# Kernel optimization log

Measured on AMD Instinct MI355X. Metric: run time of the kernel, lower is better.

The kernel has to match this reference:

```python
import jax, jax.numpy as jnp
import numpy as np

F_DIM = 2
L_LEVELS = 16
N_MIN, N_MAX = 16, 2048
_B = np.exp((np.log(N_MAX) - np.log(N_MIN)) / (L_LEVELS - 1))
NL = np.array([int(np.floor(N_MIN * _B ** l)) for l in range(L_LEVELS)], dtype=np.float32)
T_SIZE = 2 ** 19
AABB = 3.0
N_PTS = 262144
N_FREQ_DIR = 4  # direction PE frequencies -> 3 + 3*2*4 = 27 dims (matches color_MLP input 16+27)
PIS = np.array([1, 2654435761, 805459861], dtype=np.uint32)
# 8 cube-corner offsets; order matches the torch vertex enumeration
OFFS = np.array([[0,0,0],[1,0,0],[0,1,0],[1,1,0],[0,0,1],[1,0,1],[0,1,1],[1,1,1]], dtype=np.float32)


def _hash_encode(xn, tables):
    # xn: [N,3] normalized positions in ~[0,1); tables: [L,T,F]
    Ns = jnp.asarray(NL)                                   # [L]
    scaled = xn[None, :, :] * Ns[:, None, None]            # [L,N,3]
    fl = jnp.floor(scaled)
    loc = scaled - fl                                      # [L,N,3] trilinear weights
    offs_i = jnp.asarray(OFFS, jnp.int32)                  # [8,3]
    verts = fl.astype(jnp.int32)[:, :, None, :] + offs_i[None, None]   # [L,N,8,3]
    v = verts.astype(jnp.uint32)
    pis = jnp.asarray(PIS)
    h = ((v[..., 0] * pis[0]) ^ (v[..., 1] * pis[1]) ^ (v[..., 2] * pis[2])) % jnp.uint32(T_SIZE)
    idx = h.astype(jnp.int32)                              # [L,N,8]
    corner = jax.vmap(lambda t, i: t[i])(tables, idx)      # [L,N,8,F] hashed gather
    offs = jnp.asarray(OFFS)                               # [8,3]
    w = jnp.prod(offs[None, None] * loc[:, :, None, :] + (1.0 - offs[None, None]) * (1.0 - loc[:, :, None, :]), axis=-1)  # [L,N,8]
    feats = jnp.einsum('lnc,lncf->lnf', w, corner)         # [L,N,F]
    N = xn.shape[0]
    return feats.transpose(1, 0, 2).reshape(N, L_LEVELS * F_DIM)  # [N, L*F]


def _pos_enc_dir(d):
    outs = [d]
    for j in range(N_FREQ_DIR):
        outs.append(jnp.sin((2.0 ** j) * d))
        outs.append(jnp.cos((2.0 ** j) * d))
    return jnp.concatenate(outs, axis=1)                   # [N,27]


def setup_inputs() -> dict:
    key = jax.random.key(0)
    ks = jax.random.split(key, 12)
    x = jax.random.normal(ks[0], (N_PTS, 3), jnp.float32)
    d = jax.random.normal(ks[1], (N_PTS, 3), jnp.float32)
    tables = (jax.random.uniform(ks[2], (L_LEVELS, T_SIZE, F_DIM), jnp.float32) * 2.0 - 1.0) * 1e-4
    def lin(k, fi, fo):
        return jax.random.normal(k, (fi, fo), jnp.float32) * (1.0 / np.sqrt(fi))
    return {
        'x': x, 'd': d, 'tables': tables,
        'dW1': lin(ks[3], 32, 64), 'db1': jnp.zeros((64,), jnp.float32),
        'dW2': lin(ks[4], 64, 16), 'db2': jnp.zeros((16,), jnp.float32),
        'cW1': lin(ks[5], 43, 64), 'cb1': jnp.zeros((64,), jnp.float32),
        'cW2': lin(ks[6], 64, 64), 'cb2': jnp.zeros((64,), jnp.float32),
        'cW3': lin(ks[7], 64, 3), 'cb3': jnp.zeros((3,), jnp.float32),
    }


def reference(x, d, tables, dW1, db1, dW2, db2, cW1, cb1, cW2, cb2, cW3, cb3):
    xn = x / AABB
    mask = (jnp.abs(xn[:, 0]) < 0.5) & (jnp.abs(xn[:, 1]) < 0.5) & (jnp.abs(xn[:, 2]) < 0.5)
    xn = xn + 0.5
    feats = _hash_encode(xn, tables)                        # [N,32]
    h = jnp.maximum(feats @ dW1 + db1, 0.0) @ dW2 + db2     # [N,16]
    d_enc = _pos_enc_dir(d)                                 # [N,27]
    ch = jnp.concatenate([h, d_enc], axis=1)                # [N,43]
    ch = jnp.maximum(ch @ cW1 + cb1, 0.0)
    ch = jnp.maximum(ch @ cW2 + cb2, 0.0)
    rgb = jax.nn.sigmoid(ch @ cW3 + cb3)                    # [N,3]
    sigma = jnp.where(mask, h[:, 0], jnp.float32(-100000.0))
    rgb = jnp.where(mask[:, None], rgb, 0.0)
    return rgb, jnp.exp(sigma)
```

## Files before the change

kernel.cpp:

```cpp
#include <hip/hip_runtime.h>

#define NPTS 262144
#define HP1 2654435761u
#define HP2 805459861u
#define TMASK 0x7FFFFu

typedef __attribute__((ext_vector_type(8))) short short8;
typedef __attribute__((ext_vector_type(4))) float f32x4;
typedef unsigned short ushort_t;
typedef unsigned int uint_t;

#define MFMA(a, b, c) __builtin_amdgcn_mfma_f32_16x16x32_bf16((a), (b), (c), 0, 0, 0)

__device__ __forceinline__ ushort_t f2bf(float f) {
    uint_t u = __float_as_uint(f);
    return (ushort_t)((u + 0x7FFFu + ((u >> 16) & 1u)) >> 16);
}
__device__ __forceinline__ float sigmoidf_fast(float v) {
    return 1.0f / (1.0f + __expf(-v));
}

#define DOFF0 0
#define DOFF1 4913
#define DOFF2 17080
#define DOFF3 46871
#define DOFF4 126378
#define DTOT  331757
#define DENSE_BLOCKS 1296

#define WS_DN_OFF (16u * 1024u * 1024u)
#define WS_WF_OFF (22u * 1024u * 1024u)

#define OFF_DW1 0
#define OFF_DW2 2048
#define OFF_CW1 3072
#define OFF_CW2 7168
#define OFF_CW3 11264
#define WF_TOTAL 12288
#define PREP_BLOCKS 48

extern "C" __global__ void ngp_predense(
    const float* __restrict__ dW1, const float* __restrict__ dW2,
    const float* __restrict__ cW1, const float* __restrict__ cW2,
    const float* __restrict__ cW3, ushort_t* __restrict__ wf,
    const float* __restrict__ tbl, f32x4* __restrict__ dense)
{
    if (blockIdx.x < PREP_BLOCKS) {
        const int e = blockIdx.x * 256 + (int)threadIdx.x;
        if (e >= WF_TOTAL) return;
        const float* W; int base, NT, KR, NR;
        if (e < OFF_DW2)      { W = dW1; base = OFF_DW1; NT = 4; KR = 32; NR = 64; }
        else if (e < OFF_CW1) { W = dW2; base = OFF_DW2; NT = 1; KR = 64; NR = 16; }
        else if (e < OFF_CW2) { W = cW1; base = OFF_CW1; NT = 4; KR = 43; NR = 64; }
        else if (e < OFF_CW3) { W = cW2; base = OFF_CW2; NT = 4; KR = 64; NR = 64; }
        else                  { W = cW3; base = OFF_CW3; NT = 1; KR = 64; NR = 3;  }
        const int r = e - base;
        const int frag = r >> 9;
        const int lane = (r >> 3) & 63;
        const int j = r & 7;
        const int kc = frag / NT, nt = frag % NT;
        const int k = kc * 32 + ((lane >> 4) << 3) + j;
        const int n = nt * 16 + (lane & 15);
        const float v = (k < KR && n < NR) ? W[k * NR + n] : 0.0f;
        wf[e] = f2bf(v);
        return;
    }
    const int e = (blockIdx.x - PREP_BLOCKS) * 256 + (int)threadIdx.x;
    if (e >= DTOT) return;
    int l, base, dim;
    if (e < DOFF1)      { l = 0; base = DOFF0; dim = 17; }
    else if (e < DOFF2) { l = 1; base = DOFF1; dim = 23; }
    else if (e < DOFF3) { l = 2; base = DOFF2; dim = 31; }
    else if (e < DOFF4) { l = 3; base = DOFF3; dim = 43; }
    else                { l = 4; base = DOFF4; dim = 59; }
    const int r = e - base;
    const int v0 = r % dim;
    const int t  = r / dim;
    const int v1 = t % dim;
    const int v2 = t / dim;
    const float2* tp = (const float2*)tbl + ((size_t)l << 19);
    const unsigned hy = (unsigned)v1 * HP1;
    const unsigned hz = (unsigned)v2 * HP2;
    const unsigned h0 = ((unsigned)v0 ^ hy ^ hz) & TMASK;
    const unsigned h1 = (((unsigned)v0 + 1u) ^ hy ^ hz) & TMASK;
    const float2 c0 = tp[h0];
    const float2 c1 = tp[h1];
    dense[e] = (f32x4){c0.x, c0.y, c1.x, c1.y};
}

extern "C" __global__ void __launch_bounds__(256) ngp_encode(
    const float* __restrict__ xin, const float* __restrict__ tbl,
    const f32x4* __restrict__ dense, uint_t* __restrict__ feats)
{
    const int b  = blockIdx.x;
    const int l  = b >> 10;
    const int pt = ((b & 1023) << 8) + (int)threadIdx.x;

    static const float NLs[16] = {16.f, 22.f, 30.f, 42.f, 58.f, 80.f, 111.f, 153.f,
                                  212.f, 294.f, 406.f, 561.f, 776.f, 1072.f, 1482.f, 2048.f};
    static const int DDIM[5] = {17, 23, 31, 43, 59};
    static const int DOFFS[5] = {DOFF0, DOFF1, DOFF2, DOFF3, DOFF4};

    const float x0 = xin[3 * pt + 0];
    const float x1 = xin[3 * pt + 1];
    const float x2 = xin[3 * pt + 2];
    const bool msk = (fabsf(x0) < 1.5f) & (fabsf(x1) < 1.5f) & (fabsf(x2) < 1.5f);
    if (!msk) return;

    const float nl = NLs[l];
    const float s0 = (x0 / 3.0f + 0.5f) * nl;
    const float s1 = (x1 / 3.0f + 0.5f) * nl;
    const float s2 = (x2 / 3.0f + 0.5f) * nl;
    const float f0 = floorf(s0), f1 = floorf(s1), f2 = floorf(s2);
    const float l0 = s0 - f0, l1 = s1 - f1, l2 = s2 - f2;
    const float m0 = 1.0f - l0, m1 = 1.0f - l1, m2 = 1.0f - l2;

    float a = 0.0f, bb = 0.0f;

    if (l < 5) {
        const int dim = DDIM[l];
        const f32x4* dp = dense + DOFFS[l];
        const int idx = ((int)f2 * dim + (int)f1) * dim + (int)f0;
        const f32x4 C00 = dp[idx];
        const f32x4 C10 = dp[idx + dim];
        const f32x4 C01 = dp[idx + dim * dim];
        const f32x4 C11 = dp[idx + dim * dim + dim];
        float w;
        w = m1 * m2; a = fmaf(m0 * w, C00[0], a); bb = fmaf(m0 * w, C00[1], bb);
                     a = fmaf(l0 * w, C00[2], a); bb = fmaf(l0 * w, C00[3], bb);
        w = l1 * m2; a = fmaf(m0 * w, C10[0], a); bb = fmaf(m0 * w, C10[1], bb);
                     a = fmaf(l0 * w, C10[2], a); bb = fmaf(l0 * w, C10[3], bb);
        w = m1 * l2; a = fmaf(m0 * w, C01[0], a); bb = fmaf(m0 * w, C01[1], bb);
                     a = fmaf(l0 * w, C01[2], a); bb = fmaf(l0 * w, C01[3], bb);
        w = l1 * l2; a = fmaf(m0 * w, C11[0], a); bb = fmaf(m0 * w, C11[1], bb);
                     a = fmaf(l0 * w, C11[2], a); bb = fmaf(l0 * w, C11[3], bb);
    } else {
        const float2* tp = (const float2*)tbl + ((size_t)l << 19);
        const unsigned va0 = (unsigned)(int)f0, vb0 = va0 + 1u;
        const unsigned va1 = (unsigned)(int)f1 * HP1, vb1 = va1 + HP1;
        const unsigned va2 = (unsigned)(int)f2 * HP2, vb2 = va2 + HP2;
        const float2 c0 = tp[(va0 ^ va1 ^ va2) & TMASK];
        const float2 c1 = tp[(vb0 ^ va1 ^ va2) & TMASK];
        const float2 c2 = tp[(va0 ^ vb1 ^ va2) & TMASK];
        const float2 c3 = tp[(vb0 ^ vb1 ^ va2) & TMASK];
        const float2 c4 = tp[(va0 ^ va1 ^ vb2) & TMASK];
        const float2 c5 = tp[(vb0 ^ va1 ^ vb2) & TMASK];
        const float2 c6 = tp[(va0 ^ vb1 ^ vb2) & TMASK];
        const float2 c7 = tp[(vb0 ^ vb1 ^ vb2) & TMASK];
        float w;
        w = m1 * m2; a = fmaf(m0 * w, c0.x, a); bb = fmaf(m0 * w, c0.y, bb);
                     a = fmaf(l0 * w, c1.x, a); bb = fmaf(l0 * w, c1.y, bb);
        w = l1 * m2; a = fmaf(m0 * w, c2.x, a); bb = fmaf(m0 * w, c2.y, bb);
                     a = fmaf(l0 * w, c3.x, a); bb = fmaf(l0 * w, c3.y, bb);
        w = m1 * l2; a = fmaf(m0 * w, c4.x, a); bb = fmaf(m0 * w, c4.y, bb);
                     a = fmaf(l0 * w, c5.x, a); bb = fmaf(l0 * w, c5.y, bb);
        w = l1 * l2; a = fmaf(m0 * w, c6.x, a); bb = fmaf(m0 * w, c6.y, bb);
                     a = fmaf(l0 * w, c7.x, a); bb = fmaf(l0 * w, c7.y, bb);
    }

    feats[(size_t)l * NPTS + pt] = (uint_t)f2bf(a) | ((uint_t)f2bf(bb) << 16);
}

extern "C" __global__ void __launch_bounds__(64) ngp_mlp(
    const float* __restrict__ xin, const float* __restrict__ din,
    const uint_t* __restrict__ featsbf, const ushort_t* __restrict__ wf,
    const float* __restrict__ db1, const float* __restrict__ db2,
    const float* __restrict__ cb1, const float* __restrict__ cb2,
    const float* __restrict__ cb3,
    float* __restrict__ out)
{
    __shared__ short act[4096];
    __shared__ float mk[64];

    const int lane = (int)threadIdx.x;
    const int lrow = lane & 15;
    const int lq   = lane >> 4;
    const int ptb  = blockIdx.x * 64;
    const int p    = ptb + lane;
    char* Ab = (char*)&act[0];

#define LDSA(mt, kc) (*reinterpret_cast<const short8*>(Ab + ((((mt) * 16 + lrow) * 128 + (kc) * 64 + lq * 16) ^ ((lrow & 7) << 4))))
#define LOADB(off)   (*reinterpret_cast<const short8*>(wf + (off) + lane * 8))
#define STB16(row, col, val) *reinterpret_cast<ushort_t*>(Ab + ((((row) * 128 + (col) * 2)) ^ (((row) & 7) << 4))) = (val)

    const float x0 = xin[3 * p + 0];
    const float x1 = xin[3 * p + 1];
    const float x2 = xin[3 * p + 2];
    const bool msk = (fabsf(x0) < 1.5f) & (fabsf(x1) < 1.5f) & (fabsf(x2) < 1.5f);
    mk[lane] = msk ? 1.0f : 0.0f;

    uint_t u[16];
    #pragma unroll
    for (int l = 0; l < 16; ++l) u[l] = featsbf[(size_t)l * NPTS + p];
    #pragma unroll
    for (int c = 0; c < 4; ++c) {
        short8 v;
        #pragma unroll
        for (int q = 0; q < 4; ++q) {
            v[2 * q + 0] = (short)(u[4 * c + q] & 0xFFFFu);
            v[2 * q + 1] = (short)(u[4 * c + q] >> 16);
        }
        const int byte = (lane * 128 + 16 * c) ^ ((lane & 7) << 4);
        *reinterpret_cast<short8*>(Ab + byte) = v;
    }
    const float d0v = din[3 * p + 0];
    const float d1v = din[3 * p + 1];
    const float d2v = din[3 * p + 2];

    __syncthreads();

    f32x4 acc[4][4];
    #pragma unroll
    for (int nt = 0; nt < 4; ++nt) {
        const float b = db1[nt * 16 + lrow];
        #pragma unroll
        for (int mt = 0; mt < 4; ++mt) acc[mt][nt] = (f32x4){b, b, b, b};
    }
    {
        short8 a0 = LDSA(0, 0), a1 = LDSA(1, 0), a2 = LDSA(2, 0), a3 = LDSA(3, 0);
        #pragma unroll
        for (int nt = 0; nt < 4; ++nt) {
            const short8 B = LOADB(OFF_DW1 + nt * 512);
            acc[0][nt] = MFMA(a0, B, acc[0][nt]);
            acc[1][nt] = MFMA(a1, B, acc[1][nt]);
            acc[2][nt] = MFMA(a2, B, acc[2][nt]);
            acc[3][nt] = MFMA(a3, B, acc[3][nt]);
        }
    }
    __syncthreads();
    #pragma unroll
    for (int mt = 0; mt < 4; ++mt)
        #pragma unroll
        for (int nt = 0; nt < 4; ++nt)
            #pragma unroll
            for (int r = 0; r < 4; ++r) {
                const int row = mt * 16 + lq * 4 + r;
                STB16(row, nt * 16 + lrow, f2bf(fmaxf(acc[mt][nt][r], 0.0f)));
            }
    __syncthreads();

    f32x4 hD[4];
    {
        const float b = db2[lrow];
        #pragma unroll
        for (int mt = 0; mt < 4; ++mt) hD[mt] = (f32x4){b, b, b, b};
        #pragma unroll
        for (int kc = 0; kc < 2; ++kc) {
            const short8 B = LOADB(OFF_DW2 + kc * 512);
            #pragma unroll
            for (int mt = 0; mt < 4; ++mt) hD[mt] = MFMA(LDSA(mt, kc), B, hD[mt]);
        }
    }
    __syncthreads();

    if (lrow == 0) {
        #pragma unroll
        for (int mt = 0; mt < 4; ++mt)
            #pragma unroll
            for (int r = 0; r < 4; ++r) {
                const int row = mt * 16 + lq * 4 + r;
                out[3 * NPTS + ptb + row] = (mk[row] != 0.0f) ? __expf(hD[mt][r]) : 0.0f;
            }
    }
    #pragma unroll
    for (int mt = 0; mt < 4; ++mt)
        #pragma unroll
        for (int r = 0; r < 4; ++r) {
            const int row = mt * 16 + lq * 4 + r;
            STB16(row, lrow, f2bf(hD[mt][r]));
        }
    {
        ushort_t t[48];
        t[0] = f2bf(d0v); t[1] = f2bf(d1v); t[2] = f2bf(d2v);
        #pragma unroll
        for (int j = 0; j < 4; ++j) {
            const float s = (float)(1 << j);
            t[3 + 6 * j + 0] = f2bf(__sinf(s * d0v));
            t[3 + 6 * j + 1] = f2bf(__sinf(s * d1v));
            t[3 + 6 * j + 2] = f2bf(__sinf(s * d2v));
            t[3 + 6 * j + 3] = f2bf(__cosf(s * d0v));
            t[3 + 6 * j + 4] = f2bf(__cosf(s * d1v));
            t[3 + 6 * j + 5] = f2bf(__cosf(s * d2v));
        }
        #pragma unroll
        for (int i = 27; i < 48; ++i) t[i] = 0;
        #pragma unroll
        for (int c = 0; c < 6; ++c) {
            short8 v;
            #pragma unroll
            for (int j = 0; j < 8; ++j) v[j] = (short)t[8 * c + j];
            const int byte = (lane * 128 + 32 + 16 * c) ^ ((lane & 7) << 4);
            *reinterpret_cast<short8*>(Ab + byte) = v;
        }
    }
    __syncthreads();

    #pragma unroll
    for (int nt = 0; nt < 4; ++nt) {
        const float b = cb1[nt * 16 + lrow];
        #pragma unroll
        for (int mt = 0; mt < 4; ++mt) acc[mt][nt] = (f32x4){b, b, b, b};
    }
    #pragma unroll
    for (int kc = 0; kc < 2; ++kc) {
        short8 a0 = LDSA(0, kc), a1 = LDSA(1, kc), a2 = LDSA(2, kc), a3 = LDSA(3, kc);
        #pragma unroll
        for (int nt = 0; nt < 4; ++nt) {
            const short8 B = LOADB(OFF_CW1 + (kc * 4 + nt) * 512);
            acc[0][nt] = MFMA(a0, B, acc[0][nt]);
            acc[1][nt] = MFMA(a1, B, acc[1][nt]);
            acc[2][nt] = MFMA(a2, B, acc[2][nt]);
            acc[3][nt] = MFMA(a3, B, acc[3][nt]);
        }
    }
    __syncthreads();
    #pragma unroll
    for (int mt = 0; mt < 4; ++mt)
        #pragma unroll
        for (int nt = 0; nt < 4; ++nt)
            #pragma unroll
            for (int r = 0; r < 4; ++r) {
                const int row = mt * 16 + lq * 4 + r;
                STB16(row, nt * 16 + lrow, f2bf(fmaxf(acc[mt][nt][r], 0.0f)));
            }
    __syncthreads();

    #pragma unroll
    for (int nt = 0; nt < 4; ++nt) {
        const float b = cb2[nt * 16 + lrow];
        #pragma unroll
        for (int mt = 0; mt < 4; ++mt) acc[mt][nt] = (f32x4){b, b, b, b};
    }
    #pragma unroll
    for (int kc = 0; kc < 2; ++kc) {
        short8 a0 = LDSA(0, kc), a1 = LDSA(1, kc), a2 = LDSA(2, kc), a3 = LDSA(3, kc);
        #pragma unroll
        for (int nt = 0; nt < 4; ++nt) {
            const short8 B = LOADB(OFF_CW2 + (kc * 4 + nt) * 512);
            acc[0][nt] = MFMA(a0, B, acc[0][nt]);
            acc[1][nt] = MFMA(a1, B, acc[1][nt]);
            acc[2][nt] = MFMA(a2, B, acc[2][nt]);
            acc[3][nt] = MFMA(a3, B, acc[3][nt]);
        }
    }
    __syncthreads();
    #pragma unroll
    for (int mt = 0; mt < 4; ++mt)
        #pragma unroll
        for (int nt = 0; nt < 4; ++nt)
            #pragma unroll
            for (int r = 0; r < 4; ++r) {
                const int row = mt * 16 + lq * 4 + r;
                STB16(row, nt * 16 + lrow, f2bf(fmaxf(acc[mt][nt][r], 0.0f)));
            }
    __syncthreads();

    f32x4 rD[4];
    {
        const float b = (lrow < 3) ? cb3[lrow] : 0.0f;
        #pragma unroll
        for (int mt = 0; mt < 4; ++mt) rD[mt] = (f32x4){b, b, b, b};
        #pragma unroll
        for (int kc = 0; kc < 2; ++kc) {
            const short8 B = LOADB(OFF_CW3 + kc * 512);
            #pragma unroll
            for (int mt = 0; mt < 4; ++mt) rD[mt] = MFMA(LDSA(mt, kc), B, rD[mt]);
        }
    }
    if (lrow < 3) {
        #pragma unroll
        for (int mt = 0; mt < 4; ++mt)
            #pragma unroll
            for (int r = 0; r < 4; ++r) {
                const int row = mt * 16 + lq * 4 + r;
                out[3 * (ptb + row) + lrow] = (mk[row] != 0.0f) ? sigmoidf_fast(rD[mt][r]) : 0.0f;
            }
    }
#undef LDSA
#undef LOADB
#undef STB16
}

extern "C" void kernel_launch(void* const* d_in, const int* in_sizes, int n_in,
                              void* d_out, int out_size, void* d_ws, size_t ws_size,
                              hipStream_t stream) {
    const float* x    = (const float*)d_in[0];
    const float* d    = (const float*)d_in[1];
    const float* tbl  = (const float*)d_in[2];
    const float* dW1  = (const float*)d_in[3];
    const float* db1  = (const float*)d_in[4];
    const float* dW2  = (const float*)d_in[5];
    const float* db2  = (const float*)d_in[6];
    const float* cW1  = (const float*)d_in[7];
    const float* cb1  = (const float*)d_in[8];
    const float* cW2  = (const float*)d_in[9];
    const float* cb2  = (const float*)d_in[10];
    const float* cW3  = (const float*)d_in[11];
    const float* cb3  = (const float*)d_in[12];

    uint_t* feats = (uint_t*)d_ws;
    f32x4* dense  = (f32x4*)((char*)d_ws + WS_DN_OFF);
    ushort_t* wfr = (ushort_t*)((char*)d_ws + WS_WF_OFF);

    ngp_predense<<<PREP_BLOCKS + DENSE_BLOCKS, 256, 0, stream>>>(
        dW1, dW2, cW1, cW2, cW3, wfr, tbl, dense);
    ngp_encode<<<16 * 1024, 256, 0, stream>>>(x, tbl, dense, feats);
    ngp_mlp<<<NPTS / 64, 64, 0, stream>>>(
        x, d, feats, wfr, db1, db2, cb1, cb2, cb3, (float*)d_out);
}
```

Measured before the change: 108.3 us.

## Drop dense-grid precompute, merge weight prep into encode, shrink MLP blocks to 16 points

Removes the predense pass that built dense corner grids for the coarse levels, so every level now does eight hashed gathers directly from the table. Weight-fragment preparation is folded into extra blocks of the encode kernel, removing one kernel launch. The MLP kernel now handles 16 points per 64-thread block instead of 64, using a quarter of the LDS and registers and launching four times as many blocks. In exchange, the coarse levels do more scattered loads, and each weight fragment is reloaded once per 16 points rather than once per 64.

```diff
diff --git a/kernel.cpp b/kernel.cpp
--- a/kernel.cpp
+++ b/kernel.cpp
@@ -20,16 +20,7 @@
     return 1.0f / (1.0f + __expf(-v));
 }
 
-#define DOFF0 0
-#define DOFF1 4913
-#define DOFF2 17080
-#define DOFF3 46871
-#define DOFF4 126378
-#define DTOT  331757
-#define DENSE_BLOCKS 1296
-
-#define WS_DN_OFF (16u * 1024u * 1024u)
-#define WS_WF_OFF (22u * 1024u * 1024u)
+#define WS_WF_OFF (16u * 1024u * 1024u)
 
 #define OFF_DW1 0
 #define OFF_DW2 2048
@@ -37,16 +28,20 @@
 #define OFF_CW2 7168
 #define OFF_CW3 11264
 #define WF_TOTAL 12288
+
+#define ENC_BLOCKS 16384
 #define PREP_BLOCKS 48
 
-extern "C" __global__ void ngp_predense(
+extern "C" __global__ void __launch_bounds__(256) ngp_encode(
+    const float* __restrict__ xin, const float* __restrict__ tbl,
+    uint_t* __restrict__ feats,
     const float* __restrict__ dW1, const float* __restrict__ dW2,
     const float* __restrict__ cW1, const float* __restrict__ cW2,
-    const float* __restrict__ cW3, ushort_t* __restrict__ wf,
-    const float* __restrict__ tbl, f32x4* __restrict__ dense)
+    const float* __restrict__ cW3, ushort_t* __restrict__ wf)
 {
-    if (blockIdx.x < PREP_BLOCKS) {
-        const int e = blockIdx.x * 256 + (int)threadIdx.x;
+    const int b = blockIdx.x;
+    if (b >= ENC_BLOCKS) {
+        const int e = (b - ENC_BLOCKS) * 256 + (int)threadIdx.x;
         if (e >= WF_TOTAL) return;
         const float* W; int base, NT, KR, NR;
         if (e < OFF_DW2)      { W = dW1; base = OFF_DW1; NT = 4; KR = 32; NR = 64; }
@@ -65,41 +60,12 @@
         wf[e] = f2bf(v);
         return;
     }
-    const int e = (blockIdx.x - PREP_BLOCKS) * 256 + (int)threadIdx.x;
-    if (e >= DTOT) return;
-    int l, base, dim;
-    if (e < DOFF1)      { l = 0; base = DOFF0; dim = 17; }
-    else if (e < DOFF2) { l = 1; base = DOFF1; dim = 23; }
-    else if (e < DOFF3) { l = 2; base = DOFF2; dim = 31; }
-    else if (e < DOFF4) { l = 3; base = DOFF3; dim = 43; }
-    else                { l = 4; base = DOFF4; dim = 59; }
-    const int r = e - base;
-    const int v0 = r % dim;
-    const int t  = r / dim;
-    const int v1 = t % dim;
-    const int v2 = t / dim;
-    const float2* tp = (const float2*)tbl + ((size_t)l << 19);
-    const unsigned hy = (unsigned)v1 * HP1;
-    const unsigned hz = (unsigned)v2 * HP2;
-    const unsigned h0 = ((unsigned)v0 ^ hy ^ hz) & TMASK;
-    const unsigned h1 = (((unsigned)v0 + 1u) ^ hy ^ hz) & TMASK;
-    const float2 c0 = tp[h0];
-    const float2 c1 = tp[h1];
-    dense[e] = (f32x4){c0.x, c0.y, c1.x, c1.y};
-}
-
-extern "C" __global__ void __launch_bounds__(256) ngp_encode(
-    const float* __restrict__ xin, const float* __restrict__ tbl,
-    const f32x4* __restrict__ dense, uint_t* __restrict__ feats)
-{
-    const int b  = blockIdx.x;
+
     const int l  = b >> 10;
     const int pt = ((b & 1023) << 8) + (int)threadIdx.x;
 
     static const float NLs[16] = {16.f, 22.f, 30.f, 42.f, 58.f, 80.f, 111.f, 153.f,
                                   212.f, 294.f, 406.f, 561.f, 776.f, 1072.f, 1482.f, 2048.f};
-    static const int DDIM[5] = {17, 23, 31, 43, 59};
-    static const int DOFFS[5] = {DOFF0, DOFF1, DOFF2, DOFF3, DOFF4};
 
     const float x0 = xin[3 * pt + 0];
     const float x1 = xin[3 * pt + 1];
@@ -115,48 +81,28 @@
     const float l0 = s0 - f0, l1 = s1 - f1, l2 = s2 - f2;
     const float m0 = 1.0f - l0, m1 = 1.0f - l1, m2 = 1.0f - l2;
 
-    float a = 0.0f, bb = 0.0f;
-
-    if (l < 5) {
-        const int dim = DDIM[l];
-        const f32x4* dp = dense + DOFFS[l];
-        const int idx = ((int)f2 * dim + (int)f1) * dim + (int)f0;
-        const f32x4 C00 = dp[idx];
-        const f32x4 C10 = dp[idx + dim];
-        const f32x4 C01 = dp[idx + dim * dim];
-        const f32x4 C11 = dp[idx + dim * dim + dim];
-        float w;
-        w = m1 * m2; a = fmaf(m0 * w, C00[0], a); bb = fmaf(m0 * w, C00[1], bb);
-                     a = fmaf(l0 * w, C00[2], a); bb = fmaf(l0 * w, C00[3], bb);
-        w = l1 * m2; a = fmaf(m0 * w, C10[0], a); bb = fmaf(m0 * w, C10[1], bb);
-                     a = fmaf(l0 * w, C10[2], a); bb = fmaf(l0 * w, C10[3], bb);
-        w = m1 * l2; a = fmaf(m0 * w, C01[0], a); bb = fmaf(m0 * w, C01[1], bb);
-                     a = fmaf(l0 * w, C01[2], a); bb = fmaf(l0 * w, C01[3], bb);
-        w = l1 * l2; a = fmaf(m0 * w, C11[0], a); bb = fmaf(m0 * w, C11[1], bb);
-                     a = fmaf(l0 * w, C11[2], a); bb = fmaf(l0 * w, C11[3], bb);
-    } else {
-        const float2* tp = (const float2*)tbl + ((size_t)l << 19);
-        const unsigned va0 = (unsigned)(int)f0, vb0 = va0 + 1u;
-        const unsigned va1 = (unsigned)(int)f1 * HP1, vb1 = va1 + HP1;
-        const unsigned va2 = (unsigned)(int)f2 * HP2, vb2 = va2 + HP2;
-        const float2 c0 = tp[(va0 ^ va1 ^ va2) & TMASK];
-        const float2 c1 = tp[(vb0 ^ va1 ^ va2) & TMASK];
-        const float2 c2 = tp[(va0 ^ vb1 ^ va2) & TMASK];
-        const float2 c3 = tp[(vb0 ^ vb1 ^ va2) & TMASK];
-        const float2 c4 = tp[(va0 ^ va1 ^ vb2) & TMASK];
-        const float2 c5 = tp[(vb0 ^ va1 ^ vb2) & TMASK];
-        const float2 c6 = tp[(va0 ^ vb1 ^ vb2) & TMASK];
-        const float2 c7 = tp[(vb0 ^ vb1 ^ vb2) & TMASK];
-        float w;
-        w = m1 * m2; a = fmaf(m0 * w, c0.x, a); bb = fmaf(m0 * w, c0.y, bb);
-                     a = fmaf(l0 * w, c1.x, a); bb = fmaf(l0 * w, c1.y, bb);
-        w = l1 * m2; a = fmaf(m0 * w, c2.x, a); bb = fmaf(m0 * w, c2.y, bb);
-                     a = fmaf(l0 * w, c3.x, a); bb = fmaf(l0 * w, c3.y, bb);
-        w = m1 * l2; a = fmaf(m0 * w, c4.x, a); bb = fmaf(m0 * w, c4.y, bb);
-                     a = fmaf(l0 * w, c5.x, a); bb = fmaf(l0 * w, c5.y, bb);
-        w = l1 * l2; a = fmaf(m0 * w, c6.x, a); bb = fmaf(m0 * w, c6.y, bb);
-                     a = fmaf(l0 * w, c7.x, a); bb = fmaf(l0 * w, c7.y, bb);
-    }
+    const float2* tp = (const float2*)tbl + ((size_t)l << 19);
+    const unsigned va0 = (unsigned)(int)f0, vb0 = va0 + 1u;
+    const unsigned va1 = (unsigned)(int)f1 * HP1, vb1 = va1 + HP1;
+    const unsigned va2 = (unsigned)(int)f2 * HP2, vb2 = va2 + HP2;
+    const float2 c0 = tp[(va0 ^ va1 ^ va2) & TMASK];
+    const float2 c1 = tp[(vb0 ^ va1 ^ va2) & TMASK];
+    const float2 c2 = tp[(va0 ^ vb1 ^ va2) & TMASK];
+    const float2 c3 = tp[(vb0 ^ vb1 ^ va2) & TMASK];
+    const float2 c4 = tp[(va0 ^ va1 ^ vb2) & TMASK];
+    const float2 c5 = tp[(vb0 ^ va1 ^ vb2) & TMASK];
+    const float2 c6 = tp[(va0 ^ vb1 ^ vb2) & TMASK];
+    const float2 c7 = tp[(vb0 ^ vb1 ^ vb2) & TMASK];
+
+    float a = 0.0f, bb = 0.0f, w;
+    w = m1 * m2; a = fmaf(m0 * w, c0.x, a); bb = fmaf(m0 * w, c0.y, bb);
+                 a = fmaf(l0 * w, c1.x, a); bb = fmaf(l0 * w, c1.y, bb);
+    w = l1 * m2; a = fmaf(m0 * w, c2.x, a); bb = fmaf(m0 * w, c2.y, bb);
+                 a = fmaf(l0 * w, c3.x, a); bb = fmaf(l0 * w, c3.y, bb);
+    w = m1 * l2; a = fmaf(m0 * w, c4.x, a); bb = fmaf(m0 * w, c4.y, bb);
+                 a = fmaf(l0 * w, c5.x, a); bb = fmaf(l0 * w, c5.y, bb);
+    w = l1 * l2; a = fmaf(m0 * w, c6.x, a); bb = fmaf(m0 * w, c6.y, bb);
+                 a = fmaf(l0 * w, c7.x, a); bb = fmaf(l0 * w, c7.y, bb);
 
     feats[(size_t)l * NPTS + pt] = (uint_t)f2bf(a) | ((uint_t)f2bf(bb) << 16);
 }
@@ -169,128 +115,100 @@
     const float* __restrict__ cb3,
     float* __restrict__ out)
 {
-    __shared__ short act[4096];
-    __shared__ float mk[64];
+    __shared__ short act[1024];
+    __shared__ float mk[16];
 
     const int lane = (int)threadIdx.x;
     const int lrow = lane & 15;
     const int lq   = lane >> 4;
-    const int ptb  = blockIdx.x * 64;
-    const int p    = ptb + lane;
+    const int ptb  = blockIdx.x * 16;
     char* Ab = (char*)&act[0];
 
-#define LDSA(mt, kc) (*reinterpret_cast<const short8*>(Ab + ((((mt) * 16 + lrow) * 128 + (kc) * 64 + lq * 16) ^ ((lrow & 7) << 4))))
+#define LDSA(kc) (*reinterpret_cast<const short8*>(Ab + ((lrow * 128 + (kc) * 64 + lq * 16) ^ ((lrow & 7) << 4))))
 #define LOADB(off)   (*reinterpret_cast<const short8*>(wf + (off) + lane * 8))
 #define STB16(row, col, val) *reinterpret_cast<ushort_t*>(Ab + ((((row) * 128 + (col) * 2)) ^ (((row) & 7) << 4))) = (val)
 
-    const float x0 = xin[3 * p + 0];
-    const float x1 = xin[3 * p + 1];
-    const float x2 = xin[3 * p + 2];
-    const bool msk = (fabsf(x0) < 1.5f) & (fabsf(x1) < 1.5f) & (fabsf(x2) < 1.5f);
-    mk[lane] = msk ? 1.0f : 0.0f;
-
-    uint_t u[16];
-    #pragma unroll
-    for (int l = 0; l < 16; ++l) u[l] = featsbf[(size_t)l * NPTS + p];
-    #pragma unroll
-    for (int c = 0; c < 4; ++c) {
+    if (lane < 16) {
+        const float x0 = xin[3 * (ptb + lane) + 0];
+        const float x1 = xin[3 * (ptb + lane) + 1];
+        const float x2 = xin[3 * (ptb + lane) + 2];
+        const bool msk = (fabsf(x0) < 1.5f) & (fabsf(x1) < 1.5f) & (fabsf(x2) < 1.5f);
+        mk[lane] = msk ? 1.0f : 0.0f;
+    }
+
+    {
+        uint_t u[4];
+        #pragma unroll
+        for (int i = 0; i < 4; ++i)
+            u[i] = featsbf[(size_t)(4 * lq + i) * NPTS + ptb + lrow];
         short8 v;
         #pragma unroll
-        for (int q = 0; q < 4; ++q) {
-            v[2 * q + 0] = (short)(u[4 * c + q] & 0xFFFFu);
-            v[2 * q + 1] = (short)(u[4 * c + q] >> 16);
+        for (int i = 0; i < 4; ++i) {
+            v[2 * i + 0] = (short)(u[i] & 0xFFFFu);
+            v[2 * i + 1] = (short)(u[i] >> 16);
         }
-        const int byte = (lane * 128 + 16 * c) ^ ((lane & 7) << 4);
+        const int byte = (lrow * 128 + 16 * lq) ^ ((lrow & 7) << 4);
         *reinterpret_cast<short8*>(Ab + byte) = v;
     }
-    const float d0v = din[3 * p + 0];
-    const float d1v = din[3 * p + 1];
-    const float d2v = din[3 * p + 2];
-
-    __syncthreads();
-
-    f32x4 acc[4][4];
+    const float d0v = din[3 * (ptb + lrow) + 0];
+    const float d1v = din[3 * (ptb + lrow) + 1];
+    const float d2v = din[3 * (ptb + lrow) + 2];
+
+    __syncthreads();
+
+    f32x4 acc[4];
     #pragma unroll
     for (int nt = 0; nt < 4; ++nt) {
         const float b = db1[nt * 16 + lrow];
-        #pragma unroll
-        for (int mt = 0; mt < 4; ++mt) acc[mt][nt] = (f32x4){b, b, b, b};
-    }
-    {
-        short8 a0 = LDSA(0, 0), a1 = LDSA(1, 0), a2 = LDSA(2, 0), a3 = LDSA(3, 0);
-        #pragma unroll
-        for (int nt = 0; nt < 4; ++nt) {
-            const short8 B = LOADB(OFF_DW1 + nt * 512);
-            acc[0][nt] = MFMA(a0, B, acc[0][nt]);
-            acc[1][nt] = MFMA(a1, B, acc[1][nt]);
-            acc[2][nt] = MFMA(a2, B, acc[2][nt]);
-            acc[3][nt] = MFMA(a3, B, acc[3][nt]);
+        acc[nt] = (f32x4){b, b, b, b};
+    }
+    {
+        const short8 a0 = LDSA(0);
+        #pragma unroll
+        for (int nt = 0; nt < 4; ++nt)
+            acc[nt] = MFMA(a0, LOADB(OFF_DW1 + nt * 512), acc[nt]);
+    }
+    __syncthreads();
+    #pragma unroll
+    for (int nt = 0; nt < 4; ++nt)
+        #pragma unroll
+        for (int r = 0; r < 4; ++r)
+            STB16(lq * 4 + r, nt * 16 + lrow, f2bf(fmaxf(acc[nt][r], 0.0f)));
+    __syncthreads();
+
+    f32x4 hD;
+    {
+        const float b = db2[lrow];
+        hD = (f32x4){b, b, b, b};
+        #pragma unroll
+        for (int kc = 0; kc < 2; ++kc)
+            hD = MFMA(LDSA(kc), LOADB(OFF_DW2 + kc * 512), hD);
+    }
+    __syncthreads();
+
+    if (lrow == 0) {
+        #pragma unroll
+        for (int r = 0; r < 4; ++r) {
+            const int row = lq * 4 + r;
+            out[3 * NPTS + ptb + row] = (mk[row] != 0.0f) ? __expf(hD[r]) : 0.0f;
         }
     }
-    __syncthreads();
-    #pragma unroll
-    for (int mt = 0; mt < 4; ++mt)
-        #pragma unroll
-        for (int nt = 0; nt < 4; ++nt)
-            #pragma unroll
-            for (int r = 0; r < 4; ++r) {
-                const int row = mt * 16 + lq * 4 + r;
-                STB16(row, nt * 16 + lrow, f2bf(fmaxf(acc[mt][nt][r], 0.0f)));
+    #pragma unroll
+    for (int r = 0; r < 4; ++r)
+        STB16(lq * 4 + r, lrow, f2bf(hD[r]));
+    {
+        const float dv[3] = {d0v, d1v, d2v};
+        #pragma unroll
+        for (int i = 0; i < 12; ++i) {
+            const int e = 12 * lq + i;
+            float val = 0.0f;
+            if (e < 3) val = dv[e];
+            else if (e < 27) {
+                const int j = (e - 3) / 6, cc = (e - 3) % 6;
+                const float s = (float)(1 << j);
+                val = (cc < 3) ? __sinf(s * dv[cc]) : __cosf(s * dv[cc - 3]);
             }
-    __syncthreads();
-
-    f32x4 hD[4];
-    {
-        const float b = db2[lrow];
-        #pragma unroll
-        for (int mt = 0; mt < 4; ++mt) hD[mt] = (f32x4){b, b, b, b};
-        #pragma unroll
-        for (int kc = 0; kc < 2; ++kc) {
-            const short8 B = LOADB(OFF_DW2 + kc * 512);
-            #pragma unroll
-            for (int mt = 0; mt < 4; ++mt) hD[mt] = MFMA(LDSA(mt, kc), B, hD[mt]);
-        }
-    }
-    __syncthreads();
-
-    if (lrow == 0) {
-        #pragma unroll
-        for (int mt = 0; mt < 4; ++mt)
-            #pragma unroll
-            for (int r = 0; r < 4; ++r) {
-                const int row = mt * 16 + lq * 4 + r;
-                out[3 * NPTS + ptb + row] = (mk[row] != 0.0f) ? __expf(hD[mt][r]) : 0.0f;
-            }
-    }
-    #pragma unroll
-    for (int mt = 0; mt < 4; ++mt)
-        #pragma unroll
-        for (int r = 0; r < 4; ++r) {
-            const int row = mt * 16 + lq * 4 + r;
-            STB16(row, lrow, f2bf(hD[mt][r]));
-        }
-    {
-        ushort_t t[48];
-        t[0] = f2bf(d0v); t[1] = f2bf(d1v); t[2] = f2bf(d2v);
-        #pragma unroll
-        for (int j = 0; j < 4; ++j) {
-            const float s = (float)(1 << j);
-            t[3 + 6 * j + 0] = f2bf(__sinf(s * d0v));
-            t[3 + 6 * j + 1] = f2bf(__sinf(s * d1v));
-            t[3 + 6 * j + 2] = f2bf(__sinf(s * d2v));
-            t[3 + 6 * j + 3] = f2bf(__cosf(s * d0v));
-            t[3 + 6 * j + 4] = f2bf(__cosf(s * d1v));
-            t[3 + 6 * j + 5] = f2bf(__cosf(s * d2v));
-        }
-        #pragma unroll
-        for (int i = 27; i < 48; ++i) t[i] = 0;
-        #pragma unroll
-        for (int c = 0; c < 6; ++c) {
-            short8 v;
-            #pragma unroll
-            for (int j = 0; j < 8; ++j) v[j] = (short)t[8 * c + j];
-            const int byte = (lane * 128 + 32 + 16 * c) ^ ((lane & 7) << 4);
-            *reinterpret_cast<short8*>(Ab + byte) = v;
+            STB16(lrow, 16 + e, f2bf(val));
         }
     }
     __syncthreads();
@@ -298,83 +216,57 @@
     #pragma unroll
     for (int nt = 0; nt < 4; ++nt) {
         const float b = cb1[nt * 16 + lrow];
-        #pragma unroll
-        for (int mt = 0; mt < 4; ++mt) acc[mt][nt] = (f32x4){b, b, b, b};
+        acc[nt] = (f32x4){b, b, b, b};
     }
     #pragma unroll
     for (int kc = 0; kc < 2; ++kc) {
-        short8 a0 = LDSA(0, kc), a1 = LDSA(1, kc), a2 = LDSA(2, kc), a3 = LDSA(3, kc);
-        #pragma unroll
-        for (int nt = 0; nt < 4; ++nt) {
-            const short8 B = LOADB(OFF_CW1 + (kc * 4 + nt) * 512);
-            acc[0][nt] = MFMA(a0, B, acc[0][nt]);
-            acc[1][nt] = MFMA(a1, B, acc[1][nt]);
-            acc[2][nt] = MFMA(a2, B, acc[2][nt]);
-            acc[3][nt] = MFMA(a3, B, acc[3][nt]);
-        }
-    }
-    __syncthreads();
-    #pragma unroll
-    for (int mt = 0; mt < 4; ++mt)
+        const short8 a0 = LDSA(kc);
         #pragma unroll
         for (int nt = 0; nt < 4; ++nt)
-            #pragma unroll
-            for (int r = 0; r < 4; ++r) {
-                const int row = mt * 16 + lq * 4 + r;
-                STB16(row, nt * 16 + lrow, f2bf(fmaxf(acc[mt][nt][r], 0.0f)));
-            }
+            acc[nt] = MFMA(a0, LOADB(OFF_CW1 + (kc * 4 + nt) * 512), acc[nt]);
+    }
+    __syncthreads();
+    #pragma unroll
+    for (int nt = 0; nt < 4; ++nt)
+        #pragma unroll
+        for (int r = 0; r < 4; ++r)
+            STB16(lq * 4 + r, nt * 16 + lrow, f2bf(fmaxf(acc[nt][r], 0.0f)));
     __syncthreads();
 
     #pragma unroll
     for (int nt = 0; nt < 4; ++nt) {
         const float b = cb2[nt * 16 + lrow];
-        #pragma unroll
-        for (int mt = 0; mt < 4; ++mt) acc[mt][nt] = (f32x4){b, b, b, b};
+        acc[nt] = (f32x4){b, b, b, b};
     }
     #pragma unroll
     for (int kc = 0; kc < 2; ++kc) {
-        short8 a0 = LDSA(0, kc), a1 = LDSA(1, kc), a2 = LDSA(2, kc), a3 = LDSA(3, kc);
-        #pragma unroll
-        for (int nt = 0; nt < 4; ++nt) {
-            const short8 B = LOADB(OFF_CW2 + (kc * 4 + nt) * 512);
-            acc[0][nt] = MFMA(a0, B, acc[0][nt]);
-            acc[1][nt] = MFMA(a1, B, acc[1][nt]);
-            acc[2][nt] = MFMA(a2, B, acc[2][nt]);
-            acc[3][nt] = MFMA(a3, B, acc[3][nt]);
+        const short8 a0 = LDSA(kc);
+        #pragma unroll
+        for (int nt = 0; nt < 4; ++nt)
+            acc[nt] = MFMA(a0, LOADB(OFF_CW2 + (kc * 4 + nt) * 512), acc[nt]);
+    }
+    __syncthreads();
+    #pragma unroll
+    for (int nt = 0; nt < 4; ++nt)
+        #pragma unroll
+        for (int r = 0; r < 4; ++r)
+            STB16(lq * 4 + r, nt * 16 + lrow, f2bf(fmaxf(acc[nt][r], 0.0f)));
+    __syncthreads();
+
+    f32x4 rD;
+    {
+        const float b = (lrow < 3) ? cb3[lrow] : 0.0f;
+        rD = (f32x4){b, b, b, b};
+        #pragma unroll
+        for (int kc = 0; kc < 2; ++kc)
+            rD = MFMA(LDSA(kc), LOADB(OFF_CW3 + kc * 512), rD);
+    }
+    if (lrow < 3) {
+        #pragma unroll
+        for (int r = 0; r < 4; ++r) {
+            const int row = lq * 4 + r;
+            out[3 * (ptb + row) + lrow] = (mk[row] != 0.0f) ? sigmoidf_fast(rD[r]) : 0.0f;
         }
-    }
-    __syncthreads();
-    #pragma unroll
-    for (int mt = 0; mt < 4; ++mt)
-        #pragma unroll
-        for (int nt = 0; nt < 4; ++nt)
-            #pragma unroll
-            for (int r = 0; r < 4; ++r) {
-                const int row = mt * 16 + lq * 4 + r;
-                STB16(row, nt * 16 + lrow, f2bf(fmaxf(acc[mt][nt][r], 0.0f)));
-            }
-    __syncthreads();
-
-    f32x4 rD[4];
-    {
-        const float b = (lrow < 3) ? cb3[lrow] : 0.0f;
-        #pragma unroll
-        for (int mt = 0; mt < 4; ++mt) rD[mt] = (f32x4){b, b, b, b};
-        #pragma unroll
-        for (int kc = 0; kc < 2; ++kc) {
-            const short8 B = LOADB(OFF_CW3 + kc * 512);
-            #pragma unroll
-            for (int mt = 0; mt < 4; ++mt) rD[mt] = MFMA(LDSA(mt, kc), B, rD[mt]);
-        }
-    }
-    if (lrow < 3) {
-        #pragma unroll
-        for (int mt = 0; mt < 4; ++mt)
-            #pragma unroll
-            for (int r = 0; r < 4; ++r) {
-                const int row = mt * 16 + lq * 4 + r;
-                out[3 * (ptb + row) + lrow] = (mk[row] != 0.0f) ? sigmoidf_fast(rD[mt][r]) : 0.0f;
-            }
     }
 #undef LDSA
 #undef LOADB
@@ -399,12 +291,10 @@
     const float* cb3  = (const float*)d_in[12];
 
     uint_t* feats = (uint_t*)d_ws;
-    f32x4* dense  = (f32x4*)((char*)d_ws + WS_DN_OFF);
     ushort_t* wfr = (ushort_t*)((char*)d_ws + WS_WF_OFF);
 
-    ngp_predense<<<PREP_BLOCKS + DENSE_BLOCKS, 256, 0, stream>>>(
-        dW1, dW2, cW1, cW2, cW3, wfr, tbl, dense);
-    ngp_encode<<<16 * 1024, 256, 0, stream>>>(x, tbl, dense, feats);
-    ngp_mlp<<<NPTS / 64, 64, 0, stream>>>(
+    ngp_encode<<<ENC_BLOCKS + PREP_BLOCKS, 256, 0, stream>>>(
+        x, tbl, feats, dW1, dW2, cW1, cW2, cW3, wfr);
+    ngp_mlp<<<NPTS / 16, 64, 0, stream>>>(
         x, d, feats, wfr, db1, db2, cb1, cb2, cb3, (float*)d_out);
 }
```

Result: slower. 113.9 us (+5.2%).
